# Kernel optimization log

Measured on AMD Instinct MI355X. Metric: run time of the kernel, lower is better.

## Reference

```python
import jax, jax.numpy as jnp
import numpy as np

INPLANES = 128
OUTPLANES = 256
N_IN = 400000      # active input voxels
M_OUT = 100000     # active output voxels (avg 4 of 8 children active)
K_OFF = 8          # 2x2x2 filter offsets
EPS = 1e-4         # scn.BatchNormalization default eps


def setup_inputs() -> dict:
    key = jax.random.key(0)
    k1, k2 = jax.random.split(key, 2)
    feats = jax.random.normal(k1, (N_IN, INPLANES), dtype=jnp.float32)
    # scn conv weight: one [Cin, Cout] matrix per filter offset, fan-in scaled init
    W = jax.random.normal(k2, (K_OFF, INPLANES, OUTPLANES), dtype=jnp.float32) / jnp.sqrt(
        float(K_OFF * INPLANES))
    gamma = jnp.ones((OUTPLANES,), dtype=jnp.float32)
    beta = jnp.zeros((OUTPLANES,), dtype=jnp.float32)

    # Rulebook: for each output voxel, the input row feeding each of the 8
    # filter offsets (stride-2/filter-2 => each input hits exactly one slot).
    # Inactive children point at padding row N_IN (zero features).
    rng = np.random.default_rng(0)
    gather_idx = np.full((M_OUT, K_OFF), N_IN, dtype=np.int32)
    active_offs = np.argsort(rng.random((M_OUT, K_OFF)), axis=1)[:, :4]  # 4 active children
    inp_ids = np.arange(N_IN, dtype=np.int32).reshape(M_OUT, 4)
    gather_idx[np.arange(M_OUT)[:, None], active_offs] = inp_ids

    return {"feats": feats, "W": W, "gamma": gamma, "beta": beta,
            "gather_idx": jnp.asarray(gather_idx)}


def reference(feats, W, gamma, beta, gather_idx):
    # pad row so inactive rulebook entries contribute zero
    feats_p = jnp.concatenate(
        [feats, jnp.zeros((1, feats.shape[1]), dtype=feats.dtype)], axis=0)
    # gather-GEMM-scatter sparse conv: sum over the 8 filter offsets
    out = jnp.zeros((gather_idx.shape[0], W.shape[2]), dtype=feats.dtype)
    for k in range(K_OFF):
        out = out + feats_p[gather_idx[:, k]] @ W[k]      # [M, Cout]
    # scn.BatchNormalization over active output sites (training-mode stats)
    mu = jnp.mean(out, axis=0)
    var = jnp.var(out, axis=0)
    y = (out - mu) * jax.lax.rsqrt(var + EPS) * gamma + beta
    return jax.nn.relu(y)
```

## Files before the change

### kernel.cpp

```cpp
#include <hip/hip_runtime.h>
#include <hip/hip_bf16.h>
#include <stdint.h>

#define CIN 128
#define COUT 256
#define NIN 400000
#define MOUT 100000
#define KOFFS 8
#define EPSV 1e-4f
#define BM 64
#define NBLK ((MOUT + BM - 1) / BM)
#define THREADS 512

typedef __attribute__((ext_vector_type(8))) short short8;
typedef __attribute__((ext_vector_type(4))) float f32x4;

__device__ __forceinline__ unsigned f2bf_u(float f) {
  union { float f; unsigned u; } v; v.f = f;
  return (v.u + 0x7FFFu + ((v.u >> 16) & 1u)) >> 16;
}

__device__ __forceinline__ unsigned pk2bf(float a, float b) {
  __hip_bfloat162 p = __float22bfloat162_rn(make_float2(a, b));
  union { __hip_bfloat162 h; unsigned u; } c; c.h = p;
  return c.u;
}

__global__ void prep_kernel(const float* __restrict__ W,
                            unsigned short* __restrict__ Wt) {
  __shared__ unsigned short t[64][257];
  const int s = blockIdx.x;
  const int tid = threadIdx.x;
  const int koff = s >> 1;
  const int cbase = (s & 1) * 64;
  const float* Wk = W + koff * (CIN * COUT);
  #pragma unroll 8
  for (int c = 0; c < 64; ++c)
    t[c][tid] = (unsigned short)f2bf_u(Wk[(cbase + c) * COUT + tid]);
  __syncthreads();
  uint4* dst = (uint4*)((char*)Wt + s * 32768);
  #pragma unroll
  for (int p = 0; p < 8; ++p) {
    int f = p * 256 + tid;
    int wn = f >> 8, rem = f & 255;
    int g = rem >> 6, l = rem & 63;
    int ks = g >> 1, ni = g & 1;
    int n = wn * 32 + ni * 16 + (l & 15);
    int cb = ks * 32 + ((l >> 4) << 3);
    uint4 w;
    w.x = (unsigned)t[cb + 0][n] | ((unsigned)t[cb + 1][n] << 16);
    w.y = (unsigned)t[cb + 2][n] | ((unsigned)t[cb + 3][n] << 16);
    w.z = (unsigned)t[cb + 4][n] | ((unsigned)t[cb + 5][n] << 16);
    w.w = (unsigned)t[cb + 6][n] | ((unsigned)t[cb + 7][n] << 16);
    dst[f] = w;
  }
}

__global__ __launch_bounds__(THREADS, 4) void conv_kernel(
    const float* __restrict__ feats,
    const unsigned short* __restrict__ Wt,
    const int* __restrict__ gidx,
    unsigned short* __restrict__ rawout,
    float* __restrict__ out32,
    float* __restrict__ partial) {
  __shared__ unsigned short Asm[257 * 128];
  __shared__ int IDXs[BM * KOFFS];

  const int tid = threadIdx.x;
  const int lane = tid & 63;
  const int wave = tid >> 6;
  const int row16 = lane & 15;
  const int quad = lane >> 4;
  const long base_m = (long)blockIdx.x * BM;
  const long in_base = 4 * base_m;
  const char* Wtc = (const char*)Wt;

  short8 bX0, bX1, bY0, bY1;
  {
    const char* bp = Wtc + (wave << 12) + (lane << 4);
    bX0 = *(const short8*)bp;
    bX1 = *(const short8*)(bp + 1024);
  }

  for (int i = tid; i < BM * KOFFS; i += THREADS) {
    long m = base_m + (i >> 3);
    int idx = (m < MOUT) ? gidx[m * KOFFS + (i & 7)] : NIN;
    long li = (long)idx - in_base;
    IDXs[i] = ((unsigned long)li > 255ul) ? 256 : (int)li;
  }
  if (tid < 16) *(uint4*)((char*)Asm + 256 * 256 + tid * 16) = make_uint4(0, 0, 0, 0);

  {
    const float4* f4 = (const float4*)feats + in_base * 32;
    float4 v[16];
    if (in_base + 256 <= NIN) {
      #pragma unroll
      for (int p = 0; p < 16; ++p) v[p] = f4[p * THREADS + tid];
    } else {
      #pragma unroll
      for (int p = 0; p < 16; ++p) {
        int j = p * THREADS + tid;
        v[p] = (in_base + (j >> 5) < NIN) ? f4[j]
                                          : make_float4(0.f, 0.f, 0.f, 0.f);
      }
    }
    #pragma unroll
    for (int p = 0; p < 16; ++p) {
      int j = p * THREADS + tid;
      int row = j >> 5, ch4 = j & 31;
      uint2 w;
      w.x = pk2bf(v[p].x, v[p].y);
      w.y = pk2bf(v[p].z, v[p].w);
      *(uint2*)((char*)Asm + row * 256 + ((ch4 * 8) ^ ((row & 15) << 4))) = w;
    }
  }
  __syncthreads();

  int lir0[8], lir1[8], lir2[8], lir3[8];
  #pragma unroll
  for (int k = 0; k < 8; ++k) {
    lir0[k] = IDXs[(row16) * 8 + k];
    lir1[k] = IDXs[(row16 + 16) * 8 + k];
    lir2[k] = IDXs[(row16 + 32) * 8 + k];
    lir3[k] = IDXs[(row16 + 48) * 8 + k];
  }

  auto AF = [&](int li, int inner) -> short8 {
    return *(const short8*)((const char*)Asm + li * 256 +
                            (inner ^ ((li & 15) << 4)));
  };

  f32x4 acc[4][2];
  #pragma unroll
  for (int mi = 0; mi < 4; ++mi)
    #pragma unroll
    for (int ni = 0; ni < 2; ++ni)
      acc[mi][ni] = (f32x4){0.f, 0.f, 0.f, 0.f};

  short8 aX0, aX1, aX2, aX3, aY0, aY1, aY2, aY3;

#define AFLD(h, d0, d1, d2, d3) {                                         \
    const int inner_ = ((((h) >> 1) & 1) << 7) + (((h) & 1) << 6) + (quad << 4); \
    const int ko_ = (h) >> 2;                                             \
    d0 = AF(lir0[ko_], inner_); d1 = AF(lir1[ko_], inner_);               \
    d2 = AF(lir2[ko_], inner_); d3 = AF(lir3[ko_], inner_); }

#define BLD(h, e0, e1) {                                                  \
    const char* bp_ = Wtc + ((h) >> 1) * 32768 + (wave << 12) +           \
                      (((h) & 1) << 11) + (lane << 4);                    \
    e0 = *(const short8*)bp_; e1 = *(const short8*)(bp_ + 1024); }

#define MFMA8(a0, a1, a2, a3, b0, b1)                                     \
    __builtin_amdgcn_s_setprio(1);                                        \
    acc[0][0] = __builtin_amdgcn_mfma_f32_16x16x32_bf16(a0, b0, acc[0][0], 0, 0, 0); \
    acc[0][1] = __builtin_amdgcn_mfma_f32_16x16x32_bf16(a0, b1, acc[0][1], 0, 0, 0); \
    acc[1][0] = __builtin_amdgcn_mfma_f32_16x16x32_bf16(a1, b0, acc[1][0], 0, 0, 0); \
    acc[1][1] = __builtin_amdgcn_mfma_f32_16x16x32_bf16(a1, b1, acc[1][1], 0, 0, 0); \
    acc[2][0] = __builtin_amdgcn_mfma_f32_16x16x32_bf16(a2, b0, acc[2][0], 0, 0, 0); \
    acc[2][1] = __builtin_amdgcn_mfma_f32_16x16x32_bf16(a2, b1, acc[2][1], 0, 0, 0); \
    acc[3][0] = __builtin_amdgcn_mfma_f32_16x16x32_bf16(a3, b0, acc[3][0], 0, 0, 0); \
    acc[3][1] = __builtin_amdgcn_mfma_f32_16x16x32_bf16(a3, b1, acc[3][1], 0, 0, 0); \
    __builtin_amdgcn_s_setprio(0);

  AFLD(0, aX0, aX1, aX2, aX3);

  #pragma unroll
  for (int hh = 0; hh < 32; hh += 2) {
    AFLD(hh + 1, aY0, aY1, aY2, aY3);
    BLD(hh + 1, bY0, bY1);
    MFMA8(aX0, aX1, aX2, aX3, bX0, bX1);
    if (hh + 2 < 32) {
      AFLD(hh + 2, aX0, aX1, aX2, aX3);
      BLD(hh + 2, bX0, bX1);
    }
    MFMA8(aY0, aY1, aY2, aY3, bY0, bY1);
  }

#undef AFLD
#undef BLD
#undef MFMA8

  float sm[2], sq[2];
  sm[0] = sm[1] = sq[0] = sq[1] = 0.f;
  #pragma unroll
  for (int mi = 0; mi < 4; ++mi) {
    #pragma unroll
    for (int rr = 0; rr < 4; ++rr) {
      long m = base_m + (mi << 4) + (quad << 2) + rr;
      bool ok = (m < MOUT);
      #pragma unroll
      for (int ni = 0; ni < 2; ++ni) {
        float v = acc[mi][ni][rr];
        int n = (wave << 5) + (ni << 4) + row16;
        if (ok) {
          if (rawout) rawout[m * COUT + n] = (unsigned short)f2bf_u(v);
          else        out32[m * COUT + n] = v;
        }
        sm[ni] += v;
        sq[ni] += v * v;
      }
    }
  }
  #pragma unroll
  for (int ni = 0; ni < 2; ++ni) {
    sm[ni] += __shfl_xor(sm[ni], 16);
    sm[ni] += __shfl_xor(sm[ni], 32);
    sq[ni] += __shfl_xor(sq[ni], 16);
    sq[ni] += __shfl_xor(sq[ni], 32);
  }
  if (quad == 0) {
    float* pb = partial + (long)blockIdx.x * 512;
    #pragma unroll
    for (int ni = 0; ni < 2; ++ni) {
      int n = (wave << 5) + (ni << 4) + row16;
      pb[n] = sm[ni];
      pb[n + 256] = sq[ni];
    }
  }
}

__global__ void reduce_kernel(const float* __restrict__ partial,
                              float* __restrict__ partial2) {
  const int j = blockIdx.x;
  const int c = threadIdx.x;
  const int b0 = j * 25;
  const int b1 = (b0 + 25 < NBLK) ? b0 + 25 : NBLK;
  float s = 0.f;
  for (int b = b0; b < b1; ++b) s += partial[(long)b * 512 + c];
  partial2[(long)j * 512 + c] = s;
}

__global__ void finalize_kernel(const float* __restrict__ partial2,
                                const float* __restrict__ gamma,
                                const float* __restrict__ beta,
                                float* __restrict__ ss) {
  int n = threadIdx.x;
  float s = 0.f, q = 0.f;
  #pragma unroll
  for (int j = 0; j < 64; ++j) {
    s += partial2[j * 512 + n];
    q += partial2[j * 512 + 256 + n];
  }
  const float inv = 1.0f / (float)MOUT;
  float mu = s * inv;
  float var = q * inv - mu * mu;
  float sc = rsqrtf(var + EPSV) * gamma[n];
  ss[n] = sc;
  ss[n + 256] = beta[n] - mu * sc;
}

__global__ void apply_bf16(const unsigned short* __restrict__ raw,
                           float* __restrict__ out,
                           const float* __restrict__ ss) {
  const int c0 = (threadIdx.x & 31) << 3;
  float scr[8], shr[8];
  #pragma unroll
  for (int j = 0; j < 8; ++j) { scr[j] = ss[c0 + j]; shr[j] = ss[c0 + j + 256]; }
  const long total = (long)MOUT * COUT / 8;
  const uint4* r4 = (const uint4*)raw;
  float4* o4 = (float4*)out;
  union { unsigned u; float f; } t;
  for (long i = (long)blockIdx.x * blockDim.x + threadIdx.x; i < total;
       i += (long)gridDim.x * blockDim.x) {
    uint4 v = r4[i];
    float4 a, b;
    t.u = v.x << 16;        a.x = t.f;
    t.u = v.x & 0xffff0000; a.y = t.f;
    t.u = v.y << 16;        a.z = t.f;
    t.u = v.y & 0xffff0000; a.w = t.f;
    t.u = v.z << 16;        b.x = t.f;
    t.u = v.z & 0xffff0000; b.y = t.f;
    t.u = v.w << 16;        b.z = t.f;
    t.u = v.w & 0xffff0000; b.w = t.f;
    a.x = fmaxf(fmaf(a.x, scr[0], shr[0]), 0.f);
    a.y = fmaxf(fmaf(a.y, scr[1], shr[1]), 0.f);
    a.z = fmaxf(fmaf(a.z, scr[2], shr[2]), 0.f);
    a.w = fmaxf(fmaf(a.w, scr[3], shr[3]), 0.f);
    b.x = fmaxf(fmaf(b.x, scr[4], shr[4]), 0.f);
    b.y = fmaxf(fmaf(b.y, scr[5], shr[5]), 0.f);
    b.z = fmaxf(fmaf(b.z, scr[6], shr[6]), 0.f);
    b.w = fmaxf(fmaf(b.w, scr[7], shr[7]), 0.f);
    o4[2 * i] = a;
    o4[2 * i + 1] = b;
  }
}

__global__ void apply_f32(float* __restrict__ out, const float* __restrict__ ss) {
  __shared__ float sc[256], sh[256];
  sc[threadIdx.x] = ss[threadIdx.x];
  sh[threadIdx.x] = ss[threadIdx.x + 256];
  __syncthreads();
  const long total = (long)MOUT * COUT / 4;
  float4* o4 = (float4*)out;
  for (long i = (long)blockIdx.x * blockDim.x + threadIdx.x; i < total;
       i += (long)gridDim.x * blockDim.x) {
    float4 v = o4[i];
    int c = (int)(i & 63) << 2;
    v.x = fmaxf(fmaf(v.x, sc[c],     sh[c]),     0.f);
    v.y = fmaxf(fmaf(v.y, sc[c + 1], sh[c + 1]), 0.f);
    v.z = fmaxf(fmaf(v.z, sc[c + 2], sh[c + 2]), 0.f);
    v.w = fmaxf(fmaf(v.w, sc[c + 3], sh[c + 3]), 0.f);
    o4[i] = v;
  }
}

extern "C" void kernel_launch(void* const* d_in, const int* in_sizes, int n_in,
                              void* d_out, int out_size, void* d_ws, size_t ws_size,
                              hipStream_t stream) {
  const float* feats = (const float*)d_in[0];
  const float* W     = (const float*)d_in[1];
  const float* gamma = (const float*)d_in[2];
  const float* beta  = (const float*)d_in[3];
  const int*   gidx  = (const int*)d_in[4];
  float* out = (float*)d_out;

  float* ss = (float*)d_ws;
  unsigned short* Wt = (unsigned short*)((char*)d_ws + 4096);
  float* partial  = (float*)((char*)d_ws + 4096 + 524288);
  float* partial2 = (float*)((char*)partial + (size_t)NBLK * 512 * 4);
  size_t raw_off = 4096 + 524288 + (size_t)NBLK * 512 * 4 + 131072;
  raw_off = (raw_off + 255) & ~(size_t)255;
  const size_t RAW_BYTES = (size_t)MOUT * COUT * 2;
  bool bf16raw = ws_size >= raw_off + RAW_BYTES;
  unsigned short* raw = bf16raw ? (unsigned short*)((char*)d_ws + raw_off) : nullptr;

  hipLaunchKernelGGL(prep_kernel, dim3(16), dim3(256), 0, stream, W, Wt);
  hipLaunchKernelGGL(conv_kernel, dim3(NBLK), dim3(THREADS), 0, stream,
                     feats, Wt, gidx, raw, bf16raw ? nullptr : out, partial);
  hipLaunchKernelGGL(reduce_kernel, dim3(64), dim3(512), 0, stream,
                     partial, partial2);
  hipLaunchKernelGGL(finalize_kernel, dim3(1), dim3(256), 0, stream,
                     partial2, gamma, beta, ss);
  if (bf16raw)
    hipLaunchKernelGGL(apply_bf16, dim3(2048), dim3(256), 0, stream, raw, out, ss);
  else
    hipLaunchKernelGGL(apply_f32, dim3(2048), dim3(256), 0, stream, out, ss);
}
```

Measured before the change: 134.4 us.

## Make conv kernel persistent and prefetch next tile's features during MFMA loop

Turns the conv kernel into a persistent grid-stride kernel with a fixed grid of 512 blocks. While the current tile's MFMAs run, it loads the next tile's input features and rulebook indices into registers, then stores them to LDS after a barrier. The aim is to hide the global-load latency of each tile's feature fetch behind compute and to cut block launch overhead. In exchange, 16 staged uint2 registers per thread add register pressure, which may lower occupancy under the 512-thread/4-block launch bound. It also adds an extra synchronization per tile.

```diff
diff --git a/kernel.cpp b/kernel.cpp
--- a/kernel.cpp
+++ b/kernel.cpp
@@ -11,6 +11,7 @@
 #define BM 64
 #define NBLK ((MOUT + BM - 1) / BM)
 #define THREADS 512
+#define PGRID 512
 
 typedef __attribute__((ext_vector_type(8))) short short8;
 typedef __attribute__((ext_vector_type(4))) float f32x4;
@@ -71,73 +72,70 @@
   const int wave = tid >> 6;
   const int row16 = lane & 15;
   const int quad = lane >> 4;
-  const long base_m = (long)blockIdx.x * BM;
-  const long in_base = 4 * base_m;
   const char* Wtc = (const char*)Wt;
-
-  short8 bX0, bX1, bY0, bY1;
-  {
-    const char* bp = Wtc + (wave << 12) + (lane << 4);
-    bX0 = *(const short8*)bp;
-    bX1 = *(const short8*)(bp + 1024);
-  }
-
-  for (int i = tid; i < BM * KOFFS; i += THREADS) {
-    long m = base_m + (i >> 3);
-    int idx = (m < MOUT) ? gidx[m * KOFFS + (i & 7)] : NIN;
-    long li = (long)idx - in_base;
-    IDXs[i] = ((unsigned long)li > 255ul) ? 256 : (int)li;
-  }
-  if (tid < 16) *(uint4*)((char*)Asm + 256 * 256 + tid * 16) = make_uint4(0, 0, 0, 0);
-
-  {
-    const float4* f4 = (const float4*)feats + in_base * 32;
-    float4 v[16];
-    if (in_base + 256 <= NIN) {
-      #pragma unroll
-      for (int p = 0; p < 16; ++p) v[p] = f4[p * THREADS + tid];
-    } else {
-      #pragma unroll
-      for (int p = 0; p < 16; ++p) {
-        int j = p * THREADS + tid;
-        v[p] = (in_base + (j >> 5) < NIN) ? f4[j]
-                                          : make_float4(0.f, 0.f, 0.f, 0.f);
-      }
-    }
-    #pragma unroll
-    for (int p = 0; p < 16; ++p) {
-      int j = p * THREADS + tid;
-      int row = j >> 5, ch4 = j & 31;
-      uint2 w;
-      w.x = pk2bf(v[p].x, v[p].y);
-      w.y = pk2bf(v[p].z, v[p].w);
-      *(uint2*)((char*)Asm + row * 256 + ((ch4 * 8) ^ ((row & 15) << 4))) = w;
-    }
-  }
-  __syncthreads();
-
-  int lir0[8], lir1[8], lir2[8], lir3[8];
-  #pragma unroll
-  for (int k = 0; k < 8; ++k) {
-    lir0[k] = IDXs[(row16) * 8 + k];
-    lir1[k] = IDXs[(row16 + 16) * 8 + k];
-    lir2[k] = IDXs[(row16 + 32) * 8 + k];
-    lir3[k] = IDXs[(row16 + 48) * 8 + k];
-  }
 
   auto AF = [&](int li, int inner) -> short8 {
     return *(const short8*)((const char*)Asm + li * 256 +
                             (inner ^ ((li & 15) << 4)));
   };
 
-  f32x4 acc[4][2];
-  #pragma unroll
-  for (int mi = 0; mi < 4; ++mi)
-    #pragma unroll
-    for (int ni = 0; ni < 2; ++ni)
-      acc[mi][ni] = (f32x4){0.f, 0.f, 0.f, 0.f};
-
-  short8 aX0, aX1, aX2, aX3, aY0, aY1, aY2, aY3;
+  long t = blockIdx.x;
+  {
+    const long base_m = t * BM;
+    const long in_base = 4 * base_m;
+    {
+      long m = base_m + (tid >> 3);
+      int idx = (m < MOUT) ? gidx[m * KOFFS + (tid & 7)] : NIN;
+      long li = (long)idx - in_base;
+      IDXs[tid] = ((unsigned long)li > 255ul) ? 256 : (int)li;
+    }
+    if (tid < 16) *(uint4*)((char*)Asm + 256 * 256 + tid * 16) = make_uint4(0, 0, 0, 0);
+    const float4* f4 = (const float4*)feats + in_base * 32;
+    #pragma unroll 4
+    for (int p = 0; p < 16; ++p) {
+      int j = p * THREADS + tid;
+      float4 vv = (in_base + (j >> 5) < NIN) ? f4[j]
+                                             : make_float4(0.f, 0.f, 0.f, 0.f);
+      int row = j >> 5, ch4 = j & 31;
+      uint2 w;
+      w.x = pk2bf(vv.x, vv.y);
+      w.y = pk2bf(vv.z, vv.w);
+      *(uint2*)((char*)Asm + row * 256 + ((ch4 * 8) ^ ((row & 15) << 4))) = w;
+    }
+  }
+  __syncthreads();
+
+  while (t < NBLK) {
+    const long base_m = t * BM;
+    const long tn = t + (long)gridDim.x;
+    const bool have_next = (tn < NBLK);
+
+    short8 bX0, bX1, bY0, bY1;
+    {
+      const char* bp = Wtc + (wave << 12) + (lane << 4);
+      bX0 = *(const short8*)bp;
+      bX1 = *(const short8*)(bp + 1024);
+    }
+
+    int lir0[8], lir1[8], lir2[8], lir3[8];
+    #pragma unroll
+    for (int k = 0; k < 8; ++k) {
+      lir0[k] = IDXs[(row16) * 8 + k];
+      lir1[k] = IDXs[(row16 + 16) * 8 + k];
+      lir2[k] = IDXs[(row16 + 32) * 8 + k];
+      lir3[k] = IDXs[(row16 + 48) * 8 + k];
+    }
+
+    f32x4 acc[4][2];
+    #pragma unroll
+    for (int mi = 0; mi < 4; ++mi)
+      #pragma unroll
+      for (int ni = 0; ni < 2; ++ni)
+        acc[mi][ni] = (f32x4){0.f, 0.f, 0.f, 0.f};
+
+    short8 aX0, aX1, aX2, aX3, aY0, aY1, aY2, aY3;
+    uint2 stw[16];
+    int idn = NIN;
 
 #define AFLD(h, d0, d1, d2, d3) {                                         \
     const int inner_ = ((((h) >> 1) & 1) << 7) + (((h) & 1) << 6) + (quad << 4); \
@@ -162,60 +160,101 @@
     acc[3][1] = __builtin_amdgcn_mfma_f32_16x16x32_bf16(a3, b1, acc[3][1], 0, 0, 0); \
     __builtin_amdgcn_s_setprio(0);
 
-  AFLD(0, aX0, aX1, aX2, aX3);
-
-  #pragma unroll
-  for (int hh = 0; hh < 32; hh += 2) {
-    AFLD(hh + 1, aY0, aY1, aY2, aY3);
-    BLD(hh + 1, bY0, bY1);
-    MFMA8(aX0, aX1, aX2, aX3, bX0, bX1);
-    if (hh + 2 < 32) {
-      AFLD(hh + 2, aX0, aX1, aX2, aX3);
-      BLD(hh + 2, bX0, bX1);
-    }
-    MFMA8(aY0, aY1, aY2, aY3, bY0, bY1);
-  }
+    AFLD(0, aX0, aX1, aX2, aX3);
+
+    #pragma unroll
+    for (int hh = 0; hh < 32; hh += 2) {
+      AFLD(hh + 1, aY0, aY1, aY2, aY3);
+      BLD(hh + 1, bY0, bY1);
+      MFMA8(aX0, aX1, aX2, aX3, bX0, bX1);
+      if (hh == 8) {
+        if (have_next) {
+          const long in_b2 = 4 * tn * BM;
+          const float4* f4 = (const float4*)feats + in_b2 * 32;
+          if (in_b2 + 256 <= (long)NIN) {
+            #pragma unroll
+            for (int p = 0; p < 16; ++p) {
+              float4 vv = f4[p * THREADS + tid];
+              stw[p].x = pk2bf(vv.x, vv.y);
+              stw[p].y = pk2bf(vv.z, vv.w);
+            }
+          } else {
+            #pragma unroll
+            for (int p = 0; p < 16; ++p) {
+              int j = p * THREADS + tid;
+              float4 vv = (in_b2 + (j >> 5) < NIN) ? f4[j]
+                                                   : make_float4(0.f, 0.f, 0.f, 0.f);
+              stw[p].x = pk2bf(vv.x, vv.y);
+              stw[p].y = pk2bf(vv.z, vv.w);
+            }
+          }
+          long m2 = tn * BM + (tid >> 3);
+          idn = (m2 < MOUT) ? gidx[m2 * KOFFS + (tid & 7)] : NIN;
+        }
+      }
+      if (hh + 2 < 32) {
+        AFLD(hh + 2, aX0, aX1, aX2, aX3);
+        BLD(hh + 2, bX0, bX1);
+      }
+      MFMA8(aY0, aY1, aY2, aY3, bY0, bY1);
+    }
 
 #undef AFLD
 #undef BLD
 #undef MFMA8
 
-  float sm[2], sq[2];
-  sm[0] = sm[1] = sq[0] = sq[1] = 0.f;
-  #pragma unroll
-  for (int mi = 0; mi < 4; ++mi) {
-    #pragma unroll
-    for (int rr = 0; rr < 4; ++rr) {
-      long m = base_m + (mi << 4) + (quad << 2) + rr;
-      bool ok = (m < MOUT);
+    float sm[2], sq[2];
+    sm[0] = sm[1] = sq[0] = sq[1] = 0.f;
+    #pragma unroll
+    for (int mi = 0; mi < 4; ++mi) {
+      #pragma unroll
+      for (int rr = 0; rr < 4; ++rr) {
+        long m = base_m + (mi << 4) + (quad << 2) + rr;
+        bool ok = (m < MOUT);
+        #pragma unroll
+        for (int ni = 0; ni < 2; ++ni) {
+          float v = acc[mi][ni][rr];
+          int n = (wave << 5) + (ni << 4) + row16;
+          if (ok) {
+            if (rawout) rawout[m * COUT + n] = (unsigned short)f2bf_u(v);
+            else        out32[m * COUT + n] = v;
+          }
+          sm[ni] += v;
+          sq[ni] += v * v;
+        }
+      }
+    }
+    #pragma unroll
+    for (int ni = 0; ni < 2; ++ni) {
+      sm[ni] += __shfl_xor(sm[ni], 16);
+      sm[ni] += __shfl_xor(sm[ni], 32);
+      sq[ni] += __shfl_xor(sq[ni], 16);
+      sq[ni] += __shfl_xor(sq[ni], 32);
+    }
+    if (quad == 0) {
+      float* pb = partial + t * 512;
       #pragma unroll
       for (int ni = 0; ni < 2; ++ni) {
-        float v = acc[mi][ni][rr];
         int n = (wave << 5) + (ni << 4) + row16;
-        if (ok) {
-          if (rawout) rawout[m * COUT + n] = (unsigned short)f2bf_u(v);
-          else        out32[m * COUT + n] = v;
-        }
-        sm[ni] += v;
-        sq[ni] += v * v;
-      }
-    }
-  }
-  #pragma unroll
-  for (int ni = 0; ni < 2; ++ni) {
-    sm[ni] += __shfl_xor(sm[ni], 16);
-    sm[ni] += __shfl_xor(sm[ni], 32);
-    sq[ni] += __shfl_xor(sq[ni], 16);
-    sq[ni] += __shfl_xor(sq[ni], 32);
-  }
-  if (quad == 0) {
-    float* pb = partial + (long)blockIdx.x * 512;
-    #pragma unroll
-    for (int ni = 0; ni < 2; ++ni) {
-      int n = (wave << 5) + (ni << 4) + row16;
-      pb[n] = sm[ni];
-      pb[n + 256] = sq[ni];
-    }
+        pb[n] = sm[ni];
+        pb[n + 256] = sq[ni];
+      }
+    }
+
+    __syncthreads();
+    if (have_next) {
+      const long in_b2 = 4 * tn * BM;
+      #pragma unroll
+      for (int p = 0; p < 16; ++p) {
+        int j = p * THREADS + tid;
+        int row = j >> 5, ch4 = j & 31;
+        *(uint2*)((char*)Asm + row * 256 + ((ch4 * 8) ^ ((row & 15) << 4))) = stw[p];
+      }
+      long li = (long)idn - in_b2;
+      IDXs[tid] = ((unsigned long)li > 255ul) ? 256 : (int)li;
+      __syncthreads();
+    }
+    t = tn;
   }
 }
 
@@ -325,7 +364,7 @@
   unsigned short* raw = bf16raw ? (unsigned short*)((char*)d_ws + raw_off) : nullptr;
 
   hipLaunchKernelGGL(prep_kernel, dim3(16), dim3(256), 0, stream, W, Wt);
-  hipLaunchKernelGGL(conv_kernel, dim3(NBLK), dim3(THREADS), 0, stream,
+  hipLaunchKernelGGL(conv_kernel, dim3(PGRID), dim3(THREADS), 0, stream,
                      feats, Wt, gidx, raw, bf16raw ? nullptr : out, partial);
   hipLaunchKernelGGL(reduce_kernel, dim3(64), dim3(512), 0, stream,
                      partial, partial2);
```

After: 425.9 us. +216.9%, slower.

## Stage fp32 features into LDS via direct global-to-LDS loads in two channel phases

Applied to the files above, without the earlier changes.

Replaces the register-staged load that converted features to bf16 before writing LDS with direct global_load_lds transfers of raw fp32 rows. The input channels are split into two 64-channel phases so the fp32 tile fits in the same LDS footprint. The bf16 conversion now happens at fragment load time, so each A element is converted several times across MFMA passes. An extra barrier pair serializes the second staging between the phases, and the per-offset index arrays are reloaded from LDS instead of kept in registers, cutting register use.

```diff
diff --git a/kernel.cpp b/kernel.cpp
--- a/kernel.cpp
+++ b/kernel.cpp
@@ -14,6 +14,8 @@
 
 typedef __attribute__((ext_vector_type(8))) short short8;
 typedef __attribute__((ext_vector_type(4))) float f32x4;
+typedef __attribute__((address_space(3))) uint32_t lds_u32;
+typedef const __attribute__((address_space(1))) uint32_t glb_u32;
 
 __device__ __forceinline__ unsigned f2bf_u(float f) {
   union { float f; unsigned u; } v; v.f = f;
@@ -63,7 +65,7 @@
     unsigned short* __restrict__ rawout,
     float* __restrict__ out32,
     float* __restrict__ partial) {
-  __shared__ unsigned short Asm[257 * 128];
+  __shared__ float As32[257 * 64];
   __shared__ int IDXs[BM * KOFFS];
 
   const int tid = threadIdx.x;
@@ -74,60 +76,46 @@
   const long base_m = (long)blockIdx.x * BM;
   const long in_base = 4 * base_m;
   const char* Wtc = (const char*)Wt;
-
-  short8 bX0, bX1, bY0, bY1;
+  const char* fsrc = (const char*)feats;
+
+  auto STAGE = [&](int ph) {
+    #pragma unroll
+    for (int p = 0; p < 8; ++p) {
+      int g = p * THREADS + tid;
+      int r = g >> 4, sl = g & 15;
+      long grow = in_base + r;
+      if (grow > NIN - 1) grow = NIN - 1;
+      const char* src = fsrc + grow * 512 + ph * 256 +
+                        ((sl ^ (r & 15)) << 4);
+      __builtin_amdgcn_global_load_lds((glb_u32*)src,
+          (lds_u32*)((char*)As32 + g * 16), 16, 0, 0);
+    }
+  };
+
+  STAGE(0);
+
   {
-    const char* bp = Wtc + (wave << 12) + (lane << 4);
-    bX0 = *(const short8*)bp;
-    bX1 = *(const short8*)(bp + 1024);
-  }
-
-  for (int i = tid; i < BM * KOFFS; i += THREADS) {
-    long m = base_m + (i >> 3);
-    int idx = (m < MOUT) ? gidx[m * KOFFS + (i & 7)] : NIN;
+    long m = base_m + (tid >> 3);
+    int idx = (m < MOUT) ? gidx[m * KOFFS + (tid & 7)] : NIN;
     long li = (long)idx - in_base;
-    IDXs[i] = ((unsigned long)li > 255ul) ? 256 : (int)li;
-  }
-  if (tid < 16) *(uint4*)((char*)Asm + 256 * 256 + tid * 16) = make_uint4(0, 0, 0, 0);
-
-  {
-    const float4* f4 = (const float4*)feats + in_base * 32;
-    float4 v[16];
-    if (in_base + 256 <= NIN) {
-      #pragma unroll
-      for (int p = 0; p < 16; ++p) v[p] = f4[p * THREADS + tid];
-    } else {
-      #pragma unroll
-      for (int p = 0; p < 16; ++p) {
-        int j = p * THREADS + tid;
-        v[p] = (in_base + (j >> 5) < NIN) ? f4[j]
-                                          : make_float4(0.f, 0.f, 0.f, 0.f);
-      }
-    }
-    #pragma unroll
-    for (int p = 0; p < 16; ++p) {
-      int j = p * THREADS + tid;
-      int row = j >> 5, ch4 = j & 31;
-      uint2 w;
-      w.x = pk2bf(v[p].x, v[p].y);
-      w.y = pk2bf(v[p].z, v[p].w);
-      *(uint2*)((char*)Asm + row * 256 + ((ch4 * 8) ^ ((row & 15) << 4))) = w;
-    }
-  }
-  __syncthreads();
-
-  int lir0[8], lir1[8], lir2[8], lir3[8];
-  #pragma unroll
-  for (int k = 0; k < 8; ++k) {
-    lir0[k] = IDXs[(row16) * 8 + k];
-    lir1[k] = IDXs[(row16 + 16) * 8 + k];
-    lir2[k] = IDXs[(row16 + 32) * 8 + k];
-    lir3[k] = IDXs[(row16 + 48) * 8 + k];
-  }
-
-  auto AF = [&](int li, int inner) -> short8 {
-    return *(const short8*)((const char*)Asm + li * 256 +
-                            (inner ^ ((li & 15) << 4)));
+    long lim = NIN - in_base;
+    if (lim > 256) lim = 256;
+    IDXs[tid] = (li < 0 || li >= lim) ? 256 : (int)li;
+  }
+  if (tid < 16) *(uint4*)((char*)As32 + 256 * 256 + tid * 16) = make_uint4(0, 0, 0, 0);
+  __syncthreads();
+
+  auto AF = [&](int li, int ks) -> short8 {
+    const int s0 = ks * 8 + quad * 2;
+    const char* base = (const char*)As32 + li * 256;
+    float4 a = *(const float4*)(base + (((s0)     ^ (li & 15)) << 4));
+    float4 b = *(const float4*)(base + (((s0 + 1) ^ (li & 15)) << 4));
+    union { unsigned u[4]; short8 s; } c;
+    c.u[0] = pk2bf(a.x, a.y);
+    c.u[1] = pk2bf(a.z, a.w);
+    c.u[2] = pk2bf(b.x, b.y);
+    c.u[3] = pk2bf(b.z, b.w);
+    return c.s;
   };
 
   f32x4 acc[4][2];
@@ -137,18 +125,16 @@
     for (int ni = 0; ni < 2; ++ni)
       acc[mi][ni] = (f32x4){0.f, 0.f, 0.f, 0.f};
 
+  int li0, li1, li2, li3;
+  auto LI_LOAD = [&](int k) {
+    li0 = IDXs[(row16) * 8 + k];
+    li1 = IDXs[(row16 + 16) * 8 + k];
+    li2 = IDXs[(row16 + 32) * 8 + k];
+    li3 = IDXs[(row16 + 48) * 8 + k];
+  };
+
   short8 aX0, aX1, aX2, aX3, aY0, aY1, aY2, aY3;
-
-#define AFLD(h, d0, d1, d2, d3) {                                         \
-    const int inner_ = ((((h) >> 1) & 1) << 7) + (((h) & 1) << 6) + (quad << 4); \
-    const int ko_ = (h) >> 2;                                             \
-    d0 = AF(lir0[ko_], inner_); d1 = AF(lir1[ko_], inner_);               \
-    d2 = AF(lir2[ko_], inner_); d3 = AF(lir3[ko_], inner_); }
-
-#define BLD(h, e0, e1) {                                                  \
-    const char* bp_ = Wtc + ((h) >> 1) * 32768 + (wave << 12) +           \
-                      (((h) & 1) << 11) + (lane << 4);                    \
-    e0 = *(const short8*)bp_; e1 = *(const short8*)(bp_ + 1024); }
+  short8 bX0, bX1, bY0, bY1;
 
 #define MFMA8(a0, a1, a2, a3, b0, b1)                                     \
     __builtin_amdgcn_s_setprio(1);                                        \
@@ -162,22 +148,42 @@
     acc[3][1] = __builtin_amdgcn_mfma_f32_16x16x32_bf16(a3, b1, acc[3][1], 0, 0, 0); \
     __builtin_amdgcn_s_setprio(0);
 
-  AFLD(0, aX0, aX1, aX2, aX3);
-
-  #pragma unroll
-  for (int hh = 0; hh < 32; hh += 2) {
-    AFLD(hh + 1, aY0, aY1, aY2, aY3);
-    BLD(hh + 1, bY0, bY1);
-    MFMA8(aX0, aX1, aX2, aX3, bX0, bX1);
-    if (hh + 2 < 32) {
-      AFLD(hh + 2, aX0, aX1, aX2, aX3);
-      BLD(hh + 2, bX0, bX1);
-    }
-    MFMA8(aY0, aY1, aY2, aY3, bY0, bY1);
-  }
-
-#undef AFLD
-#undef BLD
+  auto RUN_PHASE = [&](int ph) {
+    {
+      const char* bp = Wtc + ph * 32768 + (wave << 12) + (lane << 4);
+      bX0 = *(const short8*)bp;
+      bX1 = *(const short8*)(bp + 1024);
+    }
+    LI_LOAD(0);
+    aX0 = AF(li0, 0); aX1 = AF(li1, 0); aX2 = AF(li2, 0); aX3 = AF(li3, 0);
+    #pragma unroll
+    for (int ko = 0; ko < 8; ++ko) {
+      aY0 = AF(li0, 1); aY1 = AF(li1, 1); aY2 = AF(li2, 1); aY3 = AF(li3, 1);
+      {
+        const char* bp = Wtc + (ko * 2 + ph) * 32768 + (wave << 12) + 2048 +
+                         (lane << 4);
+        bY0 = *(const short8*)bp;
+        bY1 = *(const short8*)(bp + 1024);
+      }
+      MFMA8(aX0, aX1, aX2, aX3, bX0, bX1);
+      if (ko < 7) {
+        LI_LOAD(ko + 1);
+        aX0 = AF(li0, 0); aX1 = AF(li1, 0); aX2 = AF(li2, 0); aX3 = AF(li3, 0);
+        const char* bp = Wtc + ((ko + 1) * 2 + ph) * 32768 + (wave << 12) +
+                         (lane << 4);
+        bX0 = *(const short8*)bp;
+        bX1 = *(const short8*)(bp + 1024);
+      }
+      MFMA8(aY0, aY1, aY2, aY3, bY0, bY1);
+    }
+  };
+
+  RUN_PHASE(0);
+  __syncthreads();
+  STAGE(1);
+  __syncthreads();
+  RUN_PHASE(1);
+
 #undef MFMA8
 
   float sm[2], sq[2];
```

Result: slower. 165.4 us (+23.1%).
